# Kernel tuning notes

Measured on AMD Instinct MI355X. Metric: run time of the kernel, lower is better.

## Reference

```python
import jax, jax.numpy as jnp
import numpy as np

N_NODES = 50000
N_EDGES = 1_600_000


def gcn_conv(x, W, b, src, dst, ew, n_nodes):
    """PyG GCNConv: out = D^{-1/2}(A+I)D^{-1/2} (x W) + b, deg from edge_weight,
    self-loop weight = 1. Self-loop term handled analytically (norm = dinv[i]^2)."""
    xW = x @ W                                            # [N, F_out]
    deg = jax.ops.segment_sum(ew, dst, num_segments=n_nodes) + 1.0  # +1 self-loop
    dinv = jnp.where(deg > 0, jax.lax.rsqrt(deg), 0.0)    # [N]
    norm = dinv[src] * ew * dinv[dst]                     # [E]
    agg = jax.ops.segment_sum(norm[:, None] * xW[src], dst, num_segments=n_nodes)
    return agg + (dinv * dinv)[:, None] * xW + b


def setup_inputs() -> dict:
    key = jax.random.key(0)
    ks = jax.random.split(key, 9)
    s = lambda fi, fo: 1.0 / np.sqrt(fi)
    return {
        "x": jax.random.normal(ks[0], (N_NODES, 128), dtype=jnp.float32),
        "edge_index": jax.random.randint(ks[1], (2, N_EDGES), 0, N_NODES, dtype=jnp.int64)
        if jax.config.jax_enable_x64 else jax.random.randint(ks[1], (2, N_EDGES), 0, N_NODES, dtype=jnp.int32),
        "edge_weight": jax.random.uniform(ks[2], (N_EDGES,), dtype=jnp.float32),
        "W1": jax.random.normal(ks[3], (128, 64), dtype=jnp.float32) * s(128, 64),
        "b1": jnp.zeros((64,), dtype=jnp.float32),
        "W2": jax.random.normal(ks[4], (64, 64), dtype=jnp.float32) * s(64, 64),
        "b2": jnp.zeros((64,), dtype=jnp.float32),
        "W3": jax.random.normal(ks[5], (64, 40), dtype=jnp.float32) * s(64, 40),
        "b3": jnp.zeros((40,), dtype=jnp.float32),
    }


def reference(x, edge_index, edge_weight, W1, b1, W2, b2, W3, b3):
    src, dst = edge_index[0], edge_index[1]
    n = x.shape[0]
    h = jax.nn.relu(gcn_conv(x, W1, b1, src, dst, edge_weight, n))
    h = jax.nn.relu(gcn_conv(h, W2, b2, src, dst, edge_weight, n))
    return gcn_conv(h, W3, b3, src, dst, edge_weight, n)
```

## Files before the change

### kernel.cpp

```cpp
#include <hip/hip_runtime.h>


#define TILE 4096
#define BCAP_MAX 9216

static __device__ __forceinline__ float4 f4zero() { return make_float4(0.f, 0.f, 0.f, 0.f); }

static __device__ __forceinline__ unsigned short f2bf_rne(float x) {
    unsigned u = __float_as_uint(x);
    u += 0x7FFFu + ((u >> 16) & 1u);
    return (unsigned short)(u >> 16);
}
static __device__ __forceinline__ float bf2f(unsigned short b) {
    return __uint_as_float((unsigned)b << 16);
}

__global__ __launch_bounds__(1024) void bin_scatter_kernel(
        const int* __restrict__ src, const int* __restrict__ dst,
        const float* __restrict__ ew, int* __restrict__ bin_cursor,
        int2* __restrict__ binned, int E, int bcap) {
    __shared__ int cnt[256];
    __shared__ int scan[256];
    __shared__ int gbase[256];
    __shared__ int2 sorted[TILE];
    __shared__ unsigned char binof[TILE];
    const int tid = threadIdx.x;
    const int e0 = blockIdx.x * TILE;

    if (tid < 256) cnt[tid] = 0;
    __syncthreads();

    int mypk[4]; float myew[4]; int mybin[4]; int myrank[4]; bool myok[4];
    #pragma unroll
    for (int j = 0; j < 4; ++j) {
        int e = e0 + j * 1024 + tid;
        myok[j] = (e < E);
        if (myok[j]) {
            int d = dst[e];
            int s = src[e];
            myew[j]   = ew[e];
            mybin[j]  = d >> 8;
            mypk[j]   = (s << 8) | (d & 255);
            myrank[j] = atomicAdd(&cnt[mybin[j]], 1);
        }
    }
    __syncthreads();
    if (tid < 256) scan[tid] = cnt[tid];
    __syncthreads();
    for (int off = 1; off < 256; off <<= 1) {
        int v = 0;
        if (tid < 256) { v = scan[tid]; if (tid >= off) v += scan[tid - off]; }
        __syncthreads();
        if (tid < 256) scan[tid] = v;
        __syncthreads();
    }
    if (tid < 256 && cnt[tid] > 0)
        gbase[tid] = atomicAdd(&bin_cursor[tid], cnt[tid]);
    __syncthreads();
    #pragma unroll
    for (int j = 0; j < 4; ++j) {
        if (myok[j]) {
            int b = mybin[j];
            int slot = (scan[b] - cnt[b]) + myrank[j];
            sorted[slot] = make_int2(mypk[j], __float_as_int(myew[j]));
            binof[slot]  = (unsigned char)b;
        }
    }
    __syncthreads();
    const int total = scan[255];
    for (int i = tid; i < total; i += 1024) {
        int b = binof[i];
        int pos = gbase[b] + (i - (scan[b] - cnt[b]));
        if (pos < bcap)
            binned[(size_t)b * bcap + pos] = sorted[i];
    }
}

__global__ __launch_bounds__(1024) void bin_group_kernel(
        int2* __restrict__ binned, const int* __restrict__ bin_cursor,
        int* __restrict__ row_start, int* __restrict__ row_cnt,
        float* __restrict__ dinv, int N, int bcap) {
    __shared__ int   cntl[256];
    __shared__ float degl[256];
    __shared__ int   scan[256];
    __shared__ int   run[256];
    __shared__ int2  sorted[BCAP_MAX];
    const int b = blockIdx.x;
    const int tid = threadIdx.x;
    int n = bin_cursor[b];
    if (n > bcap) n = bcap;
    if (tid < 256) { cntl[tid] = 0; degl[tid] = 0.f; }
    __syncthreads();

    int2* seg = binned + (size_t)b * bcap;
    for (int i = tid; i < n; i += 1024) {
        int2 v = seg[i];
        int dl = v.x & 255;
        atomicAdd(&cntl[dl], 1);
        atomicAdd(&degl[dl], __int_as_float(v.y));
    }
    __syncthreads();
    if (tid < 256) scan[tid] = cntl[tid];
    __syncthreads();
    for (int off = 1; off < 256; off <<= 1) {
        int v = 0;
        if (tid < 256) { v = scan[tid]; if (tid >= off) v += scan[tid - off]; }
        __syncthreads();
        if (tid < 256) scan[tid] = v;
        __syncthreads();
    }
    if (tid < 256) {
        int ex = scan[tid] - cntl[tid];
        int d = (b << 8) + tid;
        if (d < N) {
            row_start[d] = b * bcap + ex;
            row_cnt[d]   = cntl[tid];
            dinv[d]      = rsqrtf(degl[tid] + 1.0f);
        }
        run[tid] = ex;
    }
    __syncthreads();
    for (int i = tid; i < n; i += 1024) {
        int2 v = seg[i];
        int dl = v.x & 255;
        int r = atomicAdd(&run[dl], 1);
        sorted[r] = make_int2(v.x >> 8, v.y);
    }
    __syncthreads();
    for (int i = tid; i < n; i += 1024)
        seg[i] = sorted[i];
}

template <int K, int M>
__global__ __launch_bounds__(256) void gemm_kernel(const float* __restrict__ X,
        const float* __restrict__ W, const float* __restrict__ dinv,
        unsigned short* __restrict__ Y, int N) {
    constexpr int KP = K + 4;
    __shared__ float xs[64 * KP];
    __shared__ float ws[K * M];
    const int tid = threadIdx.x;
    const int row0 = blockIdx.x * 64;

    for (int i = tid * 4; i < K * M; i += 1024)
        *(float4*)&ws[i] = *(const float4*)&W[i];

    const int nrows = min(64, N - row0);
    for (int i = tid * 4; i < 64 * K; i += 1024) {
        int r = i / K, k = i % K;
        float4 v = f4zero();
        if (r < nrows) v = *(const float4*)&X[(size_t)(row0 + r) * K + k];
        *(float4*)&xs[r * KP + k] = v;
    }
    __syncthreads();

    const int ct = tid & 15, rt = tid >> 4;
    const bool cok = (ct * 4 < M);
    float acc[4][4] = {};
    for (int k = 0; k < K; ++k) {
        float a0 = xs[(rt +  0) * KP + k];
        float a1 = xs[(rt + 16) * KP + k];
        float a2 = xs[(rt + 32) * KP + k];
        float a3 = xs[(rt + 48) * KP + k];
        float4 bv = cok ? *(const float4*)&ws[k * M + ct * 4] : f4zero();
        acc[0][0] += a0 * bv.x; acc[0][1] += a0 * bv.y; acc[0][2] += a0 * bv.z; acc[0][3] += a0 * bv.w;
        acc[1][0] += a1 * bv.x; acc[1][1] += a1 * bv.y; acc[1][2] += a1 * bv.z; acc[1][3] += a1 * bv.w;
        acc[2][0] += a2 * bv.x; acc[2][1] += a2 * bv.y; acc[2][2] += a2 * bv.z; acc[2][3] += a2 * bv.w;
        acc[3][0] += a3 * bv.x; acc[3][1] += a3 * bv.y; acc[3][2] += a3 * bv.z; acc[3][3] += a3 * bv.w;
    }
    if (cok) {
        #pragma unroll
        for (int i = 0; i < 4; ++i) {
            int r = row0 + rt + 16 * i;
            if (r < N) {
                float dd = dinv[r];
                ushort4 o;
                o.x = f2bf_rne(acc[i][0] * dd); o.y = f2bf_rne(acc[i][1] * dd);
                o.z = f2bf_rne(acc[i][2] * dd); o.w = f2bf_rne(acc[i][3] * dd);
                *(ushort4*)&Y[(size_t)r * M + ct * 4] = o;
            }
        }
    }
}

template <int F, bool RELU>
__global__ __launch_bounds__(256) void agg_kernel(const unsigned short* __restrict__ xw,
        const int2* __restrict__ csr, const int* __restrict__ row_start,
        const int* __restrict__ row_cnt, const float* __restrict__ dinv,
        const float* __restrict__ bias, float* __restrict__ out, int N) {
    int wid = (int)((blockIdx.x * blockDim.x + threadIdx.x) >> 6);
    int lane = threadIdx.x & 63;
    if (wid >= N) return;
    const int2* row = csr + row_start[wid];
    int cnt = row_cnt[wid];
    float acc0 = 0.f, acc1 = 0.f;
    for (int base = 0; base < cnt; base += 64) {
        int m = min(cnt - base, 64);
        int2 ed = make_int2(0, 0);
        if (lane < m) ed = row[base + lane];
        int j = 0;
        for (; j + 8 <= m; j += 8) {
            #pragma unroll
            for (int u = 0; u < 8; u += 2) {
                int s0 = __builtin_amdgcn_readlane(ed.x, j + u);
                int w0 = __builtin_amdgcn_readlane(ed.y, j + u);
                int s1 = __builtin_amdgcn_readlane(ed.x, j + u + 1);
                int w1 = __builtin_amdgcn_readlane(ed.y, j + u + 1);
                acc0 = fmaf(__int_as_float(w0), bf2f(xw[(size_t)s0 * F + lane]), acc0);
                acc1 = fmaf(__int_as_float(w1), bf2f(xw[(size_t)s1 * F + lane]), acc1);
            }
        }
        for (; j < m; ++j) {
            int s = __builtin_amdgcn_readlane(ed.x, j);
            int w = __builtin_amdgcn_readlane(ed.y, j);
            acc0 = fmaf(__int_as_float(w), bf2f(xw[(size_t)s * F + lane]), acc0);
        }
    }
    if (lane < F) {
        float dd = dinv[wid];
        float selfv = bf2f(xw[(size_t)wid * F + lane]);
        float acc = dd * (acc0 + acc1 + selfv) + bias[lane];
        if (RELU) acc = fmaxf(acc, 0.f);
        out[(size_t)wid * F + lane] = acc;
    }
}

static inline size_t ws_align(size_t x) { return (x + 255) & ~(size_t)255; }

extern "C" void kernel_launch(void* const* d_in, const int* in_sizes, int n_in,
                              void* d_out, int out_size, void* d_ws, size_t ws_size,
                              hipStream_t stream) {
    const float* x  = (const float*)d_in[0];
    const int*   ei = (const int*)d_in[1];
    const float* ew = (const float*)d_in[2];
    const float* W1 = (const float*)d_in[3];
    const float* b1 = (const float*)d_in[4];
    const float* W2 = (const float*)d_in[5];
    const float* b2 = (const float*)d_in[6];
    const float* W3 = (const float*)d_in[7];
    const float* b3 = (const float*)d_in[8];
    float* out = (float*)d_out;

    const int N = in_sizes[0] / 128;
    const int E = in_sizes[1] / 2;
    const int* src = ei;
    const int* dst = ei + E;
    const int nbins = (N + 255) >> 8;

    char* p = (char*)d_ws;
    size_t off = 0;
    auto alloc = [&](size_t bytes) -> char* {
        char* q = p + off;
        off = ws_align(off + bytes);
        return q;
    };
    int*   row_start  = (int*)  alloc((size_t)N * 4);
    int*   row_cnt    = (int*)  alloc((size_t)N * 4);
    float* dinv       = (float*)alloc((size_t)N * 4);
    int*   bin_cursor = (int*)  alloc((size_t)nbins * 4);
    unsigned short* xwbuf = (unsigned short*)alloc((size_t)N * 64 * 2);
    float* hbuf       = (float*)alloc((size_t)N * 64 * 4);
    size_t remain = (ws_size > off) ? (ws_size - off) : 0;
    int bcap = (int)(remain / ((size_t)nbins * 8));
    if (bcap > BCAP_MAX) bcap = BCAP_MAX;
    int2* binned = (int2*)alloc((size_t)nbins * (size_t)bcap * 8);

    hipMemsetAsync(bin_cursor, 0, (size_t)nbins * 4, stream);

    const int tb = (E + TILE - 1) / TILE;
    const int gb = (N + 63) / 64;
    const int ab = (N + 3) / 4;

    bin_scatter_kernel<<<tb, 1024, 0, stream>>>(src, dst, ew, bin_cursor, binned, E, bcap);
    bin_group_kernel<<<nbins, 1024, 0, stream>>>(binned, bin_cursor, row_start, row_cnt, dinv, N, bcap);

    gemm_kernel<128, 64><<<gb, 256, 0, stream>>>(x, W1, dinv, xwbuf, N);
    agg_kernel<64, true><<<ab, 256, 0, stream>>>(xwbuf, binned, row_start, row_cnt, dinv, b1, hbuf, N);
    gemm_kernel<64, 64><<<gb, 256, 0, stream>>>(hbuf, W2, dinv, xwbuf, N);
    agg_kernel<64, true><<<ab, 256, 0, stream>>>(xwbuf, binned, row_start, row_cnt, dinv, b2, hbuf, N);
    gemm_kernel<64, 40><<<gb, 256, 0, stream>>>(hbuf, W3, dinv, xwbuf, N);
    agg_kernel<40, false><<<ab, 256, 0, stream>>>(xwbuf, binned, row_start, row_cnt, dinv, b3, out, N);
}
```

Before: 288.2 us.

## Split wavefront into two half-waves each gathering a packed bf16 pair per lane

Reworks the aggregation kernel so each wave handles two edges at once. Each 32-lane half-wave processes a different neighbor, and each lane loads a 32-bit word holding two bf16 features instead of one 16-bit value. Partial sums from the two halves are combined with a cross-half shuffle before the self-loop, bias and ReLU epilogue, and the result is written as float2. The aim is to halve gather instructions and fill all lanes when F is 64 or less. In exchange it adds per-edge shuffles and a more complex odd-edge tail.

```diff
diff --git a/kernel.cpp b/kernel.cpp
--- a/kernel.cpp
+++ b/kernel.cpp
@@ -10,9 +10,6 @@
     unsigned u = __float_as_uint(x);
     u += 0x7FFFu + ((u >> 16) & 1u);
     return (unsigned short)(u >> 16);
-}
-static __device__ __forceinline__ float bf2f(unsigned short b) {
-    return __uint_as_float((unsigned)b << 16);
 }
 
 __global__ __launch_bounds__(1024) void bin_scatter_kernel(
@@ -187,40 +184,67 @@
         const int2* __restrict__ csr, const int* __restrict__ row_start,
         const int* __restrict__ row_cnt, const float* __restrict__ dinv,
         const float* __restrict__ bias, float* __restrict__ out, int N) {
+    constexpr int Q = F / 2;
     int wid = (int)((blockIdx.x * blockDim.x + threadIdx.x) >> 6);
     int lane = threadIdx.x & 63;
     if (wid >= N) return;
+    const int half = lane >> 5;
+    const int q = lane & 31;
+    const bool qok = (q < Q);
+    const unsigned* xw32 = (const unsigned*)xw;
     const int2* row = csr + row_start[wid];
     int cnt = row_cnt[wid];
-    float acc0 = 0.f, acc1 = 0.f;
+    float a0l = 0.f, a0h = 0.f, a1l = 0.f, a1h = 0.f;
     for (int base = 0; base < cnt; base += 64) {
         int m = min(cnt - base, 64);
         int2 ed = make_int2(0, 0);
         if (lane < m) ed = row[base + lane];
         int j = 0;
-        for (; j + 8 <= m; j += 8) {
-            #pragma unroll
-            for (int u = 0; u < 8; u += 2) {
-                int s0 = __builtin_amdgcn_readlane(ed.x, j + u);
-                int w0 = __builtin_amdgcn_readlane(ed.y, j + u);
-                int s1 = __builtin_amdgcn_readlane(ed.x, j + u + 1);
-                int w1 = __builtin_amdgcn_readlane(ed.y, j + u + 1);
-                acc0 = fmaf(__int_as_float(w0), bf2f(xw[(size_t)s0 * F + lane]), acc0);
-                acc1 = fmaf(__int_as_float(w1), bf2f(xw[(size_t)s1 * F + lane]), acc1);
+        for (; j + 4 <= m; j += 4) {
+            int   sA = __shfl(ed.x, j + half);
+            float wA = __int_as_float(__shfl(ed.y, j + half));
+            int   sB = __shfl(ed.x, j + 2 + half);
+            float wB = __int_as_float(__shfl(ed.y, j + 2 + half));
+            unsigned dA = 0, dB = 0;
+            if (qok) {
+                dA = xw32[(size_t)sA * Q + q];
+                dB = xw32[(size_t)sB * Q + q];
             }
-        }
-        for (; j < m; ++j) {
-            int s = __builtin_amdgcn_readlane(ed.x, j);
-            int w = __builtin_amdgcn_readlane(ed.y, j);
-            acc0 = fmaf(__int_as_float(w), bf2f(xw[(size_t)s * F + lane]), acc0);
-        }
-    }
-    if (lane < F) {
+            a0l = fmaf(wA, __uint_as_float(dA << 16), a0l);
+            a0h = fmaf(wA, __uint_as_float(dA & 0xFFFF0000u), a0h);
+            a1l = fmaf(wB, __uint_as_float(dB << 16), a1l);
+            a1h = fmaf(wB, __uint_as_float(dB & 0xFFFF0000u), a1h);
+        }
+        for (; j + 2 <= m; j += 2) {
+            int   sA = __shfl(ed.x, j + half);
+            float wA = __int_as_float(__shfl(ed.y, j + half));
+            unsigned dA = 0;
+            if (qok) dA = xw32[(size_t)sA * Q + q];
+            a0l = fmaf(wA, __uint_as_float(dA << 16), a0l);
+            a0h = fmaf(wA, __uint_as_float(dA & 0xFFFF0000u), a0h);
+        }
+        if (j < m) {
+            int   s = __builtin_amdgcn_readlane(ed.x, j);
+            float w = __int_as_float(__builtin_amdgcn_readlane(ed.y, j));
+            unsigned d = 0;
+            if (qok && half == 0) d = xw32[(size_t)s * Q + q];
+            if (half == 0) {
+                a1l = fmaf(w, __uint_as_float(d << 16), a1l);
+                a1h = fmaf(w, __uint_as_float(d & 0xFFFF0000u), a1h);
+            }
+        }
+    }
+    float al = a0l + a1l, ah = a0h + a1h;
+    al += __shfl_xor(al, 32);
+    ah += __shfl_xor(ah, 32);
+    if (half == 0 && qok) {
         float dd = dinv[wid];
-        float selfv = bf2f(xw[(size_t)wid * F + lane]);
-        float acc = dd * (acc0 + acc1 + selfv) + bias[lane];
-        if (RELU) acc = fmaxf(acc, 0.f);
-        out[(size_t)wid * F + lane] = acc;
+        unsigned ds = xw32[(size_t)wid * Q + q];
+        float2 bv = *(const float2*)&bias[2 * q];
+        float ol = dd * (al + __uint_as_float(ds << 16)) + bv.x;
+        float oh = dd * (ah + __uint_as_float(ds & 0xFFFF0000u)) + bv.y;
+        if (RELU) { ol = fmaxf(ol, 0.f); oh = fmaxf(oh, 0.f); }
+        *(float2*)&out[(size_t)wid * F + 2 * q] = make_float2(ol, oh);
     }
 }
 
```

Measured after the change: 291.0 us. About the same (+1.0%).

## Replace atomic bin cursors with count-scan-scatter deterministic binning

Applied to the files above, without the earlier changes.

Replaces the global atomicAdd bin cursor in the scatter pass with a separate per-tile histogram kernel and a per-bin exclusive scan over tiles, so each tile's write offsets are precomputed. This makes edge order within bins deterministic and tile-ordered, which may improve locality in later aggregation, and removes global atomic contention and the memset. The cost is two extra kernel launches and an extra read of dst.

```diff
diff --git a/kernel.cpp b/kernel.cpp
--- a/kernel.cpp
+++ b/kernel.cpp
@@ -15,17 +15,54 @@
     return __uint_as_float((unsigned)b << 16);
 }
 
+__global__ __launch_bounds__(1024) void bin_count_kernel(
+        const int* __restrict__ dst, int* __restrict__ cnt, int E, int ntiles) {
+    __shared__ int h[256];
+    const int tid = threadIdx.x;
+    const int t = blockIdx.x;
+    if (tid < 256) h[tid] = 0;
+    __syncthreads();
+    const int e0 = t * TILE;
+    #pragma unroll
+    for (int j = 0; j < 4; ++j) {
+        int e = e0 + j * 1024 + tid;
+        if (e < E) atomicAdd(&h[dst[e] >> 8], 1);
+    }
+    __syncthreads();
+    if (tid < 256) cnt[tid * ntiles + t] = h[tid];
+}
+
+__global__ __launch_bounds__(512) void bin_scan_kernel(
+        int* __restrict__ cnt, int* __restrict__ bintotal, int ntiles) {
+    __shared__ int buf[512];
+    const int b = blockIdx.x;
+    const int tid = threadIdx.x;
+    int v = (tid < ntiles) ? cnt[b * ntiles + tid] : 0;
+    buf[tid] = v;
+    __syncthreads();
+    for (int off = 1; off < 512; off <<= 1) {
+        int x = buf[tid];
+        int a = (tid >= off) ? buf[tid - off] : 0;
+        __syncthreads();
+        buf[tid] = x + a;
+        __syncthreads();
+    }
+    if (tid < ntiles) cnt[b * ntiles + tid] = buf[tid] - v;
+    if (tid == 0) bintotal[b] = buf[511];
+}
+
 __global__ __launch_bounds__(1024) void bin_scatter_kernel(
         const int* __restrict__ src, const int* __restrict__ dst,
-        const float* __restrict__ ew, int* __restrict__ bin_cursor,
-        int2* __restrict__ binned, int E, int bcap) {
+        const float* __restrict__ ew, const int* __restrict__ cntbase,
+        int2* __restrict__ binned, int E, int bcap, int ntiles) {
     __shared__ int cnt[256];
     __shared__ int scan[256];
     __shared__ int gbase[256];
     __shared__ int2 sorted[TILE];
     __shared__ unsigned char binof[TILE];
     const int tid = threadIdx.x;
-    const int e0 = blockIdx.x * TILE;
+    const int t = blockIdx.x;
+    const int e0 = t * TILE;
 
     if (tid < 256) cnt[tid] = 0;
     __syncthreads();
@@ -54,8 +91,7 @@
         if (tid < 256) scan[tid] = v;
         __syncthreads();
     }
-    if (tid < 256 && cnt[tid] > 0)
-        gbase[tid] = atomicAdd(&bin_cursor[tid], cnt[tid]);
+    if (tid < 256) gbase[tid] = cntbase[tid * ntiles + t];
     __syncthreads();
     #pragma unroll
     for (int j = 0; j < 4; ++j) {
@@ -77,7 +113,7 @@
 }
 
 __global__ __launch_bounds__(1024) void bin_group_kernel(
-        int2* __restrict__ binned, const int* __restrict__ bin_cursor,
+        int2* __restrict__ binned, const int* __restrict__ bintotal,
         int* __restrict__ row_start, int* __restrict__ row_cnt,
         float* __restrict__ dinv, int N, int bcap) {
     __shared__ int   cntl[256];
@@ -87,7 +123,7 @@
     __shared__ int2  sorted[BCAP_MAX];
     const int b = blockIdx.x;
     const int tid = threadIdx.x;
-    int n = bin_cursor[b];
+    int n = bintotal[b];
     if (n > bcap) n = bcap;
     if (tid < 256) { cntl[tid] = 0; degl[tid] = 0.f; }
     __syncthreads();
@@ -245,6 +281,7 @@
     const int* src = ei;
     const int* dst = ei + E;
     const int nbins = (N + 255) >> 8;
+    const int ntiles = (E + TILE - 1) / TILE;
 
     char* p = (char*)d_ws;
     size_t off = 0;
@@ -253,25 +290,25 @@
         off = ws_align(off + bytes);
         return q;
     };
-    int*   row_start  = (int*)  alloc((size_t)N * 4);
-    int*   row_cnt    = (int*)  alloc((size_t)N * 4);
-    float* dinv       = (float*)alloc((size_t)N * 4);
-    int*   bin_cursor = (int*)  alloc((size_t)nbins * 4);
+    int*   row_start = (int*)  alloc((size_t)N * 4);
+    int*   row_cnt   = (int*)  alloc((size_t)N * 4);
+    float* dinv      = (float*)alloc((size_t)N * 4);
+    int*   cntbase   = (int*)  alloc((size_t)256 * ntiles * 4);
+    int*   bintotal  = (int*)  alloc((size_t)256 * 4);
     unsigned short* xwbuf = (unsigned short*)alloc((size_t)N * 64 * 2);
-    float* hbuf       = (float*)alloc((size_t)N * 64 * 4);
+    float* hbuf      = (float*)alloc((size_t)N * 64 * 4);
     size_t remain = (ws_size > off) ? (ws_size - off) : 0;
     int bcap = (int)(remain / ((size_t)nbins * 8));
     if (bcap > BCAP_MAX) bcap = BCAP_MAX;
     int2* binned = (int2*)alloc((size_t)nbins * (size_t)bcap * 8);
 
-    hipMemsetAsync(bin_cursor, 0, (size_t)nbins * 4, stream);
-
-    const int tb = (E + TILE - 1) / TILE;
     const int gb = (N + 63) / 64;
     const int ab = (N + 3) / 4;
 
-    bin_scatter_kernel<<<tb, 1024, 0, stream>>>(src, dst, ew, bin_cursor, binned, E, bcap);
-    bin_group_kernel<<<nbins, 1024, 0, stream>>>(binned, bin_cursor, row_start, row_cnt, dinv, N, bcap);
+    bin_count_kernel<<<ntiles, 1024, 0, stream>>>(dst, cntbase, E, ntiles);
+    bin_scan_kernel<<<256, 512, 0, stream>>>(cntbase, bintotal, ntiles);
+    bin_scatter_kernel<<<ntiles, 1024, 0, stream>>>(src, dst, ew, cntbase, binned, E, bcap, ntiles);
+    bin_group_kernel<<<nbins, 1024, 0, stream>>>(binned, bintotal, row_start, row_cnt, dinv, N, bcap);
 
     gemm_kernel<128, 64><<<gb, 256, 0, stream>>>(x, W1, dinv, xwbuf, N);
     agg_kernel<64, true><<<ab, 256, 0, stream>>>(xwbuf, binned, row_start, row_cnt, dinv, b1, hbuf, N);
```

Result: no change. 287.0 us (-0.4%).
